# Optimization experiments

Measured on AMD Instinct MI355X. Metric: run time of the kernel, lower is better.

The kernel has to match this reference:

```python
import jax, jax.numpy as jnp
import numpy as np

ALIGNED = 7            # aligned_height == aligned_width
GRID = ALIGNED + 1     # RoIAlignFunction samples an 8x8 grid


def _roi_align_grid(features, rois, scale):
    """jwyang-style RoIAlign: one bilinear sample per grid point.
    features: [B, C, H, W]; rois: [N, 5] = (batch_idx, x1, y1, x2, y2) in image coords.
    Returns [N, C, GRID, GRID].
    """
    B, C, H, W = features.shape
    b = rois[:, 0].astype(jnp.int32)                      # [N]
    x1, y1, x2, y2 = (rois[:, i] * scale for i in (1, 2, 3, 4))
    roi_w = jnp.maximum(x2 - x1, 0.0)
    roi_h = jnp.maximum(y2 - y1, 0.0)
    bin_h = roi_h / (GRID - 1)
    bin_w = roi_w / (GRID - 1)

    g = jnp.arange(GRID, dtype=features.dtype)
    ys = y1[:, None] + g * bin_h[:, None]                 # [N, GRID]
    xs = x1[:, None] + g * bin_w[:, None]                 # [N, GRID]

    valid = ((ys >= 0) & (ys < H))[:, :, None] & ((xs >= 0) & (xs < W))[:, None, :]  # [N,G,G]

    y0 = jnp.clip(jnp.floor(ys), 0, H - 2).astype(jnp.int32)  # [N, GRID]
    x0 = jnp.clip(jnp.floor(xs), 0, W - 2).astype(jnp.int32)
    ly = (ys - y0)[:, :, None]                            # [N, GRID, 1]
    lx = (xs - x0)[:, None, :]                            # [N, 1, GRID]

    bi = b[:, None, None]                                 # [N,1,1]
    yy0, yy1 = y0[:, :, None], y0[:, :, None] + 1          # [N,GRID,1]
    xx0, xx1 = x0[:, None, :], x0[:, None, :] + 1          # [N,1,GRID]

    # Each gather -> [N, GRID, GRID, C]
    v00 = features[bi, :, yy0, xx0]
    v01 = features[bi, :, yy0, xx1]
    v10 = features[bi, :, yy1, xx0]
    v11 = features[bi, :, yy1, xx1]

    wy0, wy1 = (1.0 - ly)[..., None], ly[..., None]        # [N,GRID,1,1]
    wx0, wx1 = (1.0 - lx)[..., None], lx[..., None]        # [N,1,GRID,1]
    val = wy0 * (wx0 * v00 + wx1 * v01) + wy1 * (wx0 * v10 + wx1 * v11)
    val = jnp.where(valid[..., None], val, 0.0)            # [N,GRID,GRID,C]
    return jnp.transpose(val, (0, 3, 1, 2))                # [N,C,GRID,GRID]


def _avg_pool2x2_s1(x):
    return 0.25 * (x[..., :-1, :-1] + x[..., :-1, 1:] + x[..., 1:, :-1] + x[..., 1:, 1:])


def setup_inputs() -> dict:
    key = jax.random.key(0)
    k1, k2, k3, k4, k5 = jax.random.split(key, 5)
    B, C, H, W = 2, 256, 100, 100
    N = 2048
    img = 1600.0  # image size; feature = img * scale
    features = jax.random.normal(k1, (B, C, H, W), dtype=jnp.float32)
    bidx = jax.random.randint(k2, (N,), 0, B).astype(jnp.float32)
    xy1 = jax.random.uniform(k3, (N, 2), minval=0.0, maxval=img - 64.0)
    wh = jax.random.uniform(k4, (N, 2), minval=16.0, maxval=400.0)
    xy2 = jnp.minimum(xy1 + wh, img - 1.0)
    rois = jnp.concatenate([bidx[:, None], xy1[:, :1], xy1[:, 1:], xy2[:, :1], xy2[:, 1:]], axis=1)
    return {"features": features, "rois": rois.astype(jnp.float32), "scale": jnp.float32(0.0625)}


def reference(features, rois, scale):
    x = _roi_align_grid(features, rois, scale)   # [N, C, 8, 8]
    return _avg_pool2x2_s1(x)                    # [N, C, 7, 7]
```

## Files before the change

kernel.cpp:

```cpp
#include <hip/hip_runtime.h>
#include <hip/hip_bf16.h>
#include <stdint.h>

#define FB 2
#define FC 256
#define FH 100
#define FW 100
#define HW (FH * FW)
#define OUTHW 49
#define OUT_PER_ROI (FC * OUTHW)
#define CHUNK 32
#define NCHUNK (FC / CHUNK)

typedef unsigned int uint4v __attribute__((ext_vector_type(4)));

__global__ __launch_bounds__(256) void transpose_chw_hwc(
    const float* __restrict__ in, __hip_bfloat16* __restrict__ out) {
  __shared__ float tile[32][33];
  const int b  = blockIdx.z;
  const int c0 = blockIdx.y * 32;
  const int p0 = blockIdx.x * 32;
  const int tx = threadIdx.x;
  const int ty = threadIdx.y;
  const int p = p0 + tx;
  if (p < HW) {
#pragma unroll
    for (int cy = ty; cy < 32; cy += 8) {
      tile[cy][tx] = in[(size_t)(b * FC + c0 + cy) * HW + p];
    }
  }
  __syncthreads();
#pragma unroll
  for (int py = ty; py < 32; py += 8) {
    const int pp = p0 + py;
    if (pp < HW) {
      out[(size_t)(b * HW + pp) * FC + c0 + tx] = __float2bfloat16(tile[tx][py]);
    }
  }
}

__global__ __launch_bounds__(256) void roialign_avg_kernel(
    const __hip_bfloat16* __restrict__ F,
    const float* __restrict__ rois,
    const float* __restrict__ scale_p,
    float* __restrict__ out) {
  __shared__ float s_s[8][8][CHUNK];
  __shared__ __align__(16) float s_o[CHUNK * OUTHW];

  const int n     = blockIdx.x;
  const int chunk = blockIdx.y;
  const int tid   = threadIdx.x;
  const int c = tid & (CHUNK - 1);
  const int r = tid >> 5;

  const float scale = scale_p[0];
  const int   bi = (int)rois[n * 5 + 0];
  const float x1 = rois[n * 5 + 1] * scale;
  const float y1 = rois[n * 5 + 2] * scale;
  const float x2 = rois[n * 5 + 3] * scale;
  const float y2 = rois[n * 5 + 4] * scale;
  const float bin_w = fmaxf(x2 - x1, 0.0f) / 7.0f;
  const float bin_h = fmaxf(y2 - y1, 0.0f) / 7.0f;

  const float ysf = y1 + (float)r * bin_h;
  const bool  vy = (ysf >= 0.0f) && (ysf < (float)FH);
  const int   y0 = (int)fminf(fmaxf(floorf(ysf), 0.0f), (float)(FH - 2));
  const float ly = ysf - (float)y0;
  const float wy0 = 1.0f - ly, wy1 = ly;
  const int rowbase = (bi * HW + y0 * FW) * FC + chunk * CHUNK + c;

  float samp[8];
#pragma unroll
  for (int gx = 0; gx < 8; ++gx) {
    const float xsf = x1 + (float)gx * bin_w;
    const bool  v = vy && (xsf >= 0.0f) && (xsf < (float)FW);
    const int   x0 = (int)fminf(fmaxf(floorf(xsf), 0.0f), (float)(FW - 2));
    const float lx = xsf - (float)x0;
    const float w00 = v ? wy0 * (1.0f - lx) : 0.0f;
    const float w01 = v ? wy0 * lx          : 0.0f;
    const float w10 = v ? wy1 * (1.0f - lx) : 0.0f;
    const float w11 = v ? wy1 * lx          : 0.0f;
    const int o = rowbase + x0 * FC;
    const float v00 = __bfloat162float(F[o]);
    const float v01 = __bfloat162float(F[o + FC]);
    const float v10 = __bfloat162float(F[o + FW * FC]);
    const float v11 = __bfloat162float(F[o + FW * FC + FC]);
    samp[gx] = w00 * v00 + w01 * v01 + w10 * v10 + w11 * v11;
  }
#pragma unroll
  for (int gx = 0; gx < 8; ++gx) s_s[r][gx][c] = samp[gx];
  __syncthreads();

  if (r < 7) {
    float a[8];
#pragma unroll
    for (int j = 0; j < 8; ++j) a[j] = s_s[r][j][c] + s_s[r + 1][j][c];
    float* so = s_o + c * OUTHW + r * 7;
#pragma unroll
    for (int j = 0; j < 7; ++j) so[j] = 0.25f * (a[j] + a[j + 1]);
  }
  __syncthreads();

  const uint4v* src = (const uint4v*)s_o;
  uint4v* dst = (uint4v*)(out + (size_t)n * OUT_PER_ROI + chunk * (CHUNK * OUTHW));
#pragma unroll
  for (int k = tid; k < (CHUNK * OUTHW) / 4; k += 256) {
    __builtin_nontemporal_store(src[k], &dst[k]);
  }
}

extern "C" void kernel_launch(void* const* d_in, const int* in_sizes, int n_in,
                              void* d_out, int out_size, void* d_ws, size_t ws_size,
                              hipStream_t stream) {
  const float* features = (const float*)d_in[0];
  const float* rois     = (const float*)d_in[1];
  const float* scale    = (const float*)d_in[2];
  float* out = (float*)d_out;
  __hip_bfloat16* ft = (__hip_bfloat16*)d_ws;

  const int N = in_sizes[1] / 5;

  dim3 tb(32, 8);
  dim3 tg((HW + 31) / 32, FC / 32, FB);
  transpose_chw_hwc<<<tg, tb, 0, stream>>>(features, ft);

  roialign_avg_kernel<<<dim3(N, NCHUNK), dim3(256), 0, stream>>>(ft, rois, scale, out);
}
```

Baseline: 146.7 us.

## Process two bf16 channels per thread with 32-bit loads and 64-channel chunks

Each thread now loads packed bf16 pairs as 32-bit words and does bilinear interpolation for two adjacent channels, with the channel chunk per block doubled to 64. This halves the block count and the number of global load instructions per sample, and amortizes the ROI coordinate math over more channels. The pooling stage is remapped so 256 threads cover 64 channels by 7 rows. Shared memory use doubles per block, which may lower occupancy.

```diff
diff --git a/kernel.cpp b/kernel.cpp
--- a/kernel.cpp
+++ b/kernel.cpp
@@ -9,10 +9,11 @@
 #define HW (FH * FW)
 #define OUTHW 49
 #define OUT_PER_ROI (FC * OUTHW)
-#define CHUNK 32
+#define CHUNK 64
 #define NCHUNK (FC / CHUNK)
 
 typedef unsigned int uint4v __attribute__((ext_vector_type(4)));
+typedef float float2v __attribute__((ext_vector_type(2)));
 
 __global__ __launch_bounds__(256) void transpose_chw_hwc(
     const float* __restrict__ in, __hip_bfloat16* __restrict__ out) {
@@ -50,8 +51,8 @@
   const int n     = blockIdx.x;
   const int chunk = blockIdx.y;
   const int tid   = threadIdx.x;
-  const int c = tid & (CHUNK - 1);
-  const int r = tid >> 5;
+  const int c2 = tid & 31;
+  const int r  = tid >> 5;
 
   const float scale = scale_p[0];
   const int   bi = (int)rois[n * 5 + 0];
@@ -67,9 +68,11 @@
   const int   y0 = (int)fminf(fmaxf(floorf(ysf), 0.0f), (float)(FH - 2));
   const float ly = ysf - (float)y0;
   const float wy0 = 1.0f - ly, wy1 = ly;
-  const int rowbase = (bi * HW + y0 * FW) * FC + chunk * CHUNK + c;
+  const int rowbase = (bi * HW + y0 * FW) * FC + chunk * CHUNK + 2 * c2;
+  const uint32_t* __restrict__ Fu =
+      reinterpret_cast<const uint32_t*>(F);
 
-  float samp[8];
+  float samp0[8], samp1[8];
 #pragma unroll
   for (int gx = 0; gx < 8; ++gx) {
     const float xsf = x1 + (float)gx * bin_w;
@@ -80,24 +83,38 @@
     const float w01 = v ? wy0 * lx          : 0.0f;
     const float w10 = v ? wy1 * (1.0f - lx) : 0.0f;
     const float w11 = v ? wy1 * lx          : 0.0f;
-    const int o = rowbase + x0 * FC;
-    const float v00 = __bfloat162float(F[o]);
-    const float v01 = __bfloat162float(F[o + FC]);
-    const float v10 = __bfloat162float(F[o + FW * FC]);
-    const float v11 = __bfloat162float(F[o + FW * FC + FC]);
-    samp[gx] = w00 * v00 + w01 * v01 + w10 * v10 + w11 * v11;
+    const int o = (rowbase + x0 * FC) >> 1;
+    const uint32_t u00 = Fu[o];
+    const uint32_t u01 = Fu[o + FC / 2];
+    const uint32_t u10 = Fu[o + (FW * FC) / 2];
+    const uint32_t u11 = Fu[o + (FW * FC) / 2 + FC / 2];
+    const float a00 = __uint_as_float(u00 << 16), b00 = __uint_as_float(u00 & 0xffff0000u);
+    const float a01 = __uint_as_float(u01 << 16), b01 = __uint_as_float(u01 & 0xffff0000u);
+    const float a10 = __uint_as_float(u10 << 16), b10 = __uint_as_float(u10 & 0xffff0000u);
+    const float a11 = __uint_as_float(u11 << 16), b11 = __uint_as_float(u11 & 0xffff0000u);
+    samp0[gx] = w00 * a00 + w01 * a01 + w10 * a10 + w11 * a11;
+    samp1[gx] = w00 * b00 + w01 * b01 + w10 * b10 + w11 * b11;
   }
 #pragma unroll
-  for (int gx = 0; gx < 8; ++gx) s_s[r][gx][c] = samp[gx];
+  for (int gx = 0; gx < 8; ++gx) {
+    float2v* p = reinterpret_cast<float2v*>(&s_s[r][gx][2 * c2]);
+    float2v v2; v2.x = samp0[gx]; v2.y = samp1[gx];
+    *p = v2;
+  }
   __syncthreads();
 
-  if (r < 7) {
-    float a[8];
+  {
+    const int c = tid & 63;
+    const int r0 = tid >> 6;
 #pragma unroll
-    for (int j = 0; j < 8; ++j) a[j] = s_s[r][j][c] + s_s[r + 1][j][c];
-    float* so = s_o + c * OUTHW + r * 7;
+    for (int rp = r0; rp < 7; rp += 4) {
+      float a[8];
 #pragma unroll
-    for (int j = 0; j < 7; ++j) so[j] = 0.25f * (a[j] + a[j + 1]);
+      for (int j = 0; j < 8; ++j) a[j] = s_s[rp][j][c] + s_s[rp + 1][j][c];
+      float* so = s_o + c * OUTHW + rp * 7;
+#pragma unroll
+      for (int j = 0; j < 7; ++j) so[j] = 0.25f * (a[j] + a[j + 1]);
+    }
   }
   __syncthreads();
 
```

Result: faster. 140.8 us (-4.1%).
